# Optimization experiments

Measured on AMD Instinct MI355X. Metric: run time of the kernel, lower is better.

The kernel has to match this reference:

```python
import jax, jax.numpy as jnp
import numpy as np

DEGREE = 3        # self.degree = 3 in MGNN
K = 3             # Chebyshev/polynomial order of the GCN
BANDWIDTH = 512.0 # Gaussian kernel bandwidth (~2*d so adj spans (0,1])
B, N, D_IN = 2, 4096, 256
D_OUT = 64        # 2*D_OUT == 128 == linear output dim


def _bspline(t, degree):
    """Cox-de Boor recursive B-spline basis N_{0,degree}(t), elementwise,
    uniform knots on [0,1]. t: [B,N,N] adjacency values."""
    knots = np.linspace(0.0, 1.0, degree + 2)  # static python floats
    basis = [jnp.where((t >= knots[i]) & (t < knots[i + 1]), 1.0, 0.0).astype(t.dtype)
             for i in range(degree + 1)]
    for k in range(1, degree + 1):
        basis = [
            (t - knots[i]) / (knots[i + k] - knots[i]) * basis[i]
            + (knots[i + k + 1] - t) / (knots[i + k + 1] - knots[i + 1]) * basis[i + 1]
            for i in range(degree + 1 - k)
        ]
    return basis[0]


def _wavelet(t, degree):
    # spline wavelet: difference of dilated/shifted B-splines
    return _bspline(2.0 * t, degree) - _bspline(2.0 * t - 1.0, degree)


def _graph_construction(x, bandwidth):
    # Gaussian-kernel dense adjacency per batch element: [B,N,N], values in (0,1]
    sq = jnp.sum(x * x, axis=-1)                                   # [B,N]
    d2 = sq[:, :, None] + sq[:, None, :] - 2.0 * jnp.einsum('bnd,bmd->bnm', x, x)
    d2 = jnp.maximum(d2, 0.0)
    return jnp.exp(-d2 / bandwidth)


def _gcn(x, kernel, Wk):
    # out = sum_k (kernel^k x) W_k ; Wk: [K, D_IN, D_OUT]
    h = x
    out = jnp.einsum('bnd,do->bno', h, Wk[0])
    for k in range(1, Wk.shape[0]):
        h = jnp.einsum('bnm,bmd->bnd', kernel, h)
        out = out + jnp.einsum('bnd,do->bno', h, Wk[k])
    return out


def setup_inputs() -> dict:
    key = jax.random.key(0)
    k0, k1, k2, k3 = jax.random.split(key, 4)
    x = jax.random.normal(k0, (B, N, D_IN), dtype=jnp.float32)
    Wk = jax.random.normal(k1, (K, D_IN, D_OUT), dtype=jnp.float32) * 0.05
    W_lin = jax.random.normal(k2, (D_IN, 2 * D_OUT), dtype=jnp.float32) * 0.05
    b_lin = jnp.zeros((2 * D_OUT,), dtype=jnp.float32)
    return {"x": x, "Wk": Wk, "W_lin": W_lin, "b_lin": b_lin}


def reference(x, Wk, W_lin, b_lin):
    adj = _graph_construction(x, BANDWIDTH)       # [B,N,N]
    b_kernel = _bspline(adj, DEGREE)              # [B,N,N]
    w_kernel = _wavelet(adj, DEGREE)              # [B,N,N]
    gcn1 = _gcn(x, b_kernel, Wk)                  # [B,N,D_OUT]
    gcn2 = _gcn(x, w_kernel, Wk)                  # [B,N,D_OUT]
    akgcn = jnp.concatenate([gcn1, gcn2], axis=-1)        # [B,N,2*D_OUT]
    akgcn = jax.nn.relu(akgcn + x @ W_lin + b_lin)        # residual + relu
    return akgcn.reshape(akgcn.shape[0], -1)              # flatten last two dims
```

## Files before the change

### kernel.cpp

```cpp
#include <hip/hip_runtime.h>
#include <hip/hip_bf16.h>

typedef __hip_bfloat16 bf16;
typedef float v4f __attribute__((ext_vector_type(4)));
typedef short v8s __attribute__((ext_vector_type(8)));

typedef const __attribute__((address_space(1))) void gvoid;
typedef __attribute__((address_space(3))) void lvoid;

__device__ __forceinline__ void async16(const void* g, void* l) {
  __builtin_amdgcn_global_load_lds((gvoid*)g, (lvoid*)l, 16, 0, 0);
}

__device__ __forceinline__ unsigned short f2bf(float v) {
  __hip_bfloat16 h = __float2bfloat16(v);
  return *(unsigned short*)&h;
}
__device__ __forceinline__ float bflo(unsigned dw) {
  unsigned u = dw << 16;
  return *(float*)&u;
}
__device__ __forceinline__ float bfhi(unsigned dw) {
  unsigned u = dw & 0xffff0000u;
  return *(float*)&u;
}

__device__ __forceinline__ float b3(float u) {
  u = fminf(fmaxf(u, 0.f), 4.f);
  float t1 = fmaxf(u - 1.f, 0.f);
  float t2 = fmaxf(u - 2.f, 0.f);
  float t3 = fmaxf(u - 3.f, 0.f);
  float c0 = u * u * u;
  float c1 = t1 * t1 * t1;
  float c2 = t2 * t2 * t2;
  float c3 = t3 * t3 * t3;
  return (c0 - 4.f * c1 + 6.f * c2 - 4.f * c3) * (1.f / 6.f);
}

template <int NI, int BK>
__device__ __forceinline__ void mfma_loop(const bf16* __restrict__ A,
                                          const bf16* __restrict__ B, int lda,
                                          int ldb, int kLen, bf16* As, bf16* Bs,
                                          v4f acc[4][NI]) {
  const int tid = threadIdx.x;
  const int wave = tid >> 6;
  const int lane = tid & 63;
  const int quad = lane >> 4;
  const int r16 = lane & 15;
  const int wm = (wave >> 1) * 64;
  const int wn = (wave & 1) * (NI * 16);
  constexpr int CPR = BK / 8;
  constexpr int AQ = 128 * CPR / 256;
  constexpr int BQ = NI * 32 * CPR / 256;
  char* AsC = (char*)As;
  char* BsC = (char*)Bs;
  for (int kk = 0; kk < kLen; kk += BK) {
#pragma unroll
    for (int q = 0; q < AQ; ++q) {
      const int ch = tid + 256 * q;
      const int r = ch / CPR, c = (ch % CPR) * 8;
      async16(A + (size_t)r * lda + kk + c, AsC + q * 4096 + wave * 1024);
    }
#pragma unroll
    for (int q = 0; q < BQ; ++q) {
      const int ch = tid + 256 * q;
      const int r = ch / CPR, c = (ch % CPR) * 8;
      async16(B + (size_t)r * ldb + kk + c, BsC + q * 4096 + wave * 1024);
    }
    __syncthreads();
#pragma unroll
    for (int ks = 0; ks < BK / 32; ++ks) {
      v8s af[4], bfr[NI];
#pragma unroll
      for (int mi = 0; mi < 4; ++mi)
        af[mi] =
            *(const v8s*)(As + (wm + mi * 16 + r16) * BK + ks * 32 + quad * 8);
#pragma unroll
      for (int ni = 0; ni < NI; ++ni)
        bfr[ni] =
            *(const v8s*)(Bs + (wn + ni * 16 + r16) * BK + ks * 32 + quad * 8);
#pragma unroll
      for (int mi = 0; mi < 4; ++mi)
#pragma unroll
        for (int ni = 0; ni < NI; ++ni)
          acc[mi][ni] = __builtin_amdgcn_mfma_f32_16x16x32_bf16(
              af[mi], bfr[ni], acc[mi][ni], 0, 0, 0);
    }
    __syncthreads();
  }
}

__global__ void prep(const float* __restrict__ x, bf16* __restrict__ U,
                     float* __restrict__ sq) {
  const int n = blockIdx.x, b = blockIdx.y, t = threadIdx.x;
  const size_t row = (size_t)b * 4096 + n;
  float v = x[row * 256 + t];
  U[row * 1280 + t] = __float2bfloat16(v);
  float s = v * v;
#pragma unroll
  for (int o = 32; o > 0; o >>= 1) s += __shfl_down(s, o, 64);
  __shared__ float ls[4];
  if ((t & 63) == 0) ls[t >> 6] = s;
  __syncthreads();
  if (t == 0) sq[row] = ls[0] + ls[1] + ls[2] + ls[3];
}

__global__ void transk(const float* __restrict__ src, bf16* __restrict__ dst) {
  __shared__ float tile[64][65];
  const int z = blockIdx.z;
  const float* s = src + (size_t)z * 4096 * 256;
  bf16* d = dst + (size_t)z * 256 * 4096;
  const int n0 = blockIdx.x * 64, d0 = blockIdx.y * 64;
  const int tx = threadIdx.x & 31, ty = threadIdx.x >> 5;
#pragma unroll
  for (int i = 0; i < 8; ++i) {
    const int r = ty + i * 8;
    const float2 v = *(const float2*)(s + (size_t)(n0 + r) * 256 + d0 + tx * 2);
    tile[r][tx * 2] = v.x;
    tile[r][tx * 2 + 1] = v.y;
  }
  __syncthreads();
#pragma unroll
  for (int i = 0; i < 8; ++i) {
    const int c = ty + i * 8;
    __hip_bfloat162 p;
    p.x = __float2bfloat16(tile[tx * 2][c]);
    p.y = __float2bfloat16(tile[tx * 2 + 1][c]);
    *(__hip_bfloat162*)(d + (size_t)(d0 + c) * 4096 + n0 + tx * 2) = p;
  }
}

__global__ void wbig(const float* __restrict__ Wk, const float* __restrict__ Wl,
                     bf16* __restrict__ WbT) {
  int idx = blockIdx.x * 256 + threadIdx.x;
  if (idx >= 128 * 1280) return;
  int j = idx / 1280, k = idx % 1280;
  int o = j & 63;
  float v = 0.f;
  if (k < 256)
    v = Wk[k * 64 + o] + Wl[k * 128 + j];
  else if (k < 512)
    v = (j < 64) ? Wk[16384 + (k - 256) * 64 + o] : 0.f;
  else if (k < 768)
    v = (j < 64) ? Wk[32768 + (k - 512) * 64 + o] : 0.f;
  else if (k < 1024)
    v = (j >= 64) ? Wk[16384 + (k - 768) * 64 + o] : 0.f;
  else
    v = (j >= 64) ? Wk[32768 + (k - 1024) * 64 + o] : 0.f;
  WbT[idx] = __float2bfloat16(v);
}

__global__ __launch_bounds__(256, 2) void gemm_s(const bf16* __restrict__ U,
                                                 const float* __restrict__ sq,
                                                 bf16* __restrict__ kmat) {
  __shared__ __align__(16) bf16 As[128 * 64];
  __shared__ __align__(16) bf16 Bs[128 * 64];
  __shared__ unsigned lut[2048];
  const int tid = threadIdx.x;
  for (int i = tid; i < 2048; i += 256) {
    float t = (i + 0.5f) * (1.f / 2048.f);
    float bv = b3(4.f * t);
    float wv = b3(8.f * t) - b3(8.f * t - 4.f);
    lut[i] = (unsigned)f2bf(bv) | ((unsigned)f2bf(wv) << 16);
  }
  const int z = blockIdx.z;
  const bf16* A = U + (size_t)z * 4096 * 1280 + (size_t)blockIdx.x * 128 * 1280;
  const bf16* B = U + (size_t)z * 4096 * 1280 + (size_t)blockIdx.y * 128 * 1280;
  v4f acc[4][4];
#pragma unroll
  for (int a = 0; a < 4; ++a)
#pragma unroll
    for (int b2 = 0; b2 < 4; ++b2) acc[a][b2] = (v4f){0.f, 0.f, 0.f, 0.f};
  mfma_loop<4, 64>(A, B, 1280, 1280, 256, As, Bs, acc);
  const int wave = tid >> 6, lane = tid & 63;
  const int quad = lane >> 4, r16 = lane & 15;
  const int wm = (wave >> 1) * 64, wn = (wave & 1) * 64;
  const float* sqr = sq + (size_t)z * 4096;
  unsigned short* bk = (unsigned short*)(kmat + (size_t)(z * 2) * 4096 * 4096);
  unsigned short* wk = bk + (size_t)4096 * 4096;
  const int i0 = blockIdx.x * 128 + wm + quad * 4;
  const int j0 = blockIdx.y * 128 + wn + r16;
  const int par = lane & 1;
  const int jc = j0 - par;
  float sqj[4];
#pragma unroll
  for (int ni = 0; ni < 4; ++ni) sqj[ni] = sqr[j0 + ni * 16];
  const float c = -1.4426950408889634f / 512.f;
#pragma unroll
  for (int mi = 0; mi < 4; ++mi) {
#pragma unroll
    for (int ni = 0; ni < 4; ++ni) {
      unsigned pv[4];
#pragma unroll
      for (int r = 0; r < 4; ++r) {
        float s = acc[mi][ni][r];
        float d2 = fmaxf(sqr[i0 + mi * 16 + r] + sqj[ni] - 2.f * s, 0.f);
        float t = __builtin_amdgcn_exp2f(d2 * c);
        int idx = (int)fminf(t * 2048.f, 2047.f);
        pv[r] = lut[idx];
      }
      unsigned ov[4];
#pragma unroll
      for (int r = 0; r < 4; ++r) ov[r] = __shfl_xor((int)pv[r], 1, 64);
#pragma unroll
      for (int rr = 0; rr < 2; ++rr) {
        const int r = par * 2 + rr;
        const unsigned a = pv[r], b2 = ov[r];
        const unsigned lo = par ? b2 : a;
        const unsigned hi = par ? a : b2;
        const unsigned bkd = (lo & 0xffffu) | (hi << 16);
        const unsigned wkd = (lo >> 16) | (hi & 0xffff0000u);
        const int i = i0 + mi * 16 + r;
        const size_t off = (size_t)i * 4096 + jc + ni * 16;
        *(unsigned*)(bk + off) = bkd;
        *(unsigned*)(wk + off) = wkd;
      }
    }
  }
}

__global__ __launch_bounds__(256, 4) void gemm_h(const bf16* __restrict__ kmat,
                                                 const bf16* __restrict__ BtBase,
                                                 bf16* __restrict__ hpart,
                                                 int btShift) {
  __shared__ __align__(16) bf16 As[128 * 64];
  __shared__ __align__(16) bf16 Bs[128 * 64];
  const int bz = blockIdx.z;
  const int z = bz >> 2, split = bz & 3;
  const int kk0 = split * 1024;
  const bf16* A =
      kmat + (size_t)z * 4096 * 4096 + (size_t)blockIdx.x * 128 * 4096 + kk0;
  const bf16* B = BtBase + (size_t)(z >> btShift) * 256 * 4096 +
                  (size_t)blockIdx.y * 128 * 4096 + kk0;
  v4f acc[4][4];
#pragma unroll
  for (int a = 0; a < 4; ++a)
#pragma unroll
    for (int b2 = 0; b2 < 4; ++b2) acc[a][b2] = (v4f){0.f, 0.f, 0.f, 0.f};
  mfma_loop<4, 64>(A, B, 4096, 4096, 1024, As, Bs, acc);
  const int tid = threadIdx.x, wave = tid >> 6, lane = tid & 63;
  const int quad = lane >> 4, r16 = lane & 15;
  const int wm = (wave >> 1) * 64, wn = (wave & 1) * 64;
  bf16* H = hpart + ((size_t)split * 4 + z) * 4096 * 256;
  const int i0 = blockIdx.x * 128 + wm + quad * 4;
  const int j0 = blockIdx.y * 128 + wn + r16;
  const int par = lane & 1;
  const int jc = j0 - par;
#pragma unroll
  for (int mi = 0; mi < 4; ++mi) {
#pragma unroll
    for (int ni = 0; ni < 4; ++ni) {
      unsigned pv[4];
#pragma unroll
      for (int r = 0; r < 4; ++r) pv[r] = (unsigned)f2bf(acc[mi][ni][r]);
      unsigned ov[4];
#pragma unroll
      for (int r = 0; r < 4; ++r) ov[r] = __shfl_xor((int)pv[r], 1, 64);
#pragma unroll
      for (int rr = 0; rr < 2; ++rr) {
        const int r = par * 2 + rr;
        const unsigned a = pv[r], b2 = ov[r];
        const unsigned lo = par ? b2 : a;
        const unsigned hi = par ? a : b2;
        const int i = i0 + mi * 16 + r;
        *(unsigned*)(H + (size_t)i * 256 + jc + ni * 16) = lo | (hi << 16);
      }
    }
  }
}

__global__ void reduceT(const bf16* __restrict__ hpart, bf16* __restrict__ U,
                        bf16* __restrict__ hT, int uoffBase) {
  __shared__ float tile[64][65];
  const int z = blockIdx.z;
  const int b = z >> 1, kern = z & 1;
  const int uoff = uoffBase + kern * 512;
  const int n0 = blockIdx.x * 64, d0 = blockIdx.y * 64;
  const int tx = threadIdx.x & 31, ty = threadIdx.x >> 5;
  const size_t sstride = (size_t)4 * 4096 * 256;
  const bf16* s0 = hpart + (size_t)z * 4096 * 256;
#pragma unroll
  for (int i = 0; i < 8; ++i) {
    const int r = ty + i * 8;
    const size_t off = (size_t)(n0 + r) * 256 + d0 + tx * 2;
    float vx = 0.f, vy = 0.f;
#pragma unroll
    for (int k = 0; k < 4; ++k) {
      const unsigned dw = *(const unsigned*)(s0 + k * sstride + off);
      vx += bflo(dw);
      vy += bfhi(dw);
    }
    tile[r][tx * 2] = vx;
    tile[r][tx * 2 + 1] = vy;
    __hip_bfloat162 p;
    p.x = __float2bfloat16(vx);
    p.y = __float2bfloat16(vy);
    *(__hip_bfloat162*)(U + (size_t)(b * 4096 + n0 + r) * 1280 + uoff + d0 +
                        tx * 2) = p;
  }
  if (hT) {
    __syncthreads();
#pragma unroll
    for (int i = 0; i < 8; ++i) {
      const int c = ty + i * 8;
      __hip_bfloat162 p;
      p.x = __float2bfloat16(tile[tx * 2][c]);
      p.y = __float2bfloat16(tile[tx * 2 + 1][c]);
      *(__hip_bfloat162*)(hT + (size_t)z * 256 * 4096 + (size_t)(d0 + c) * 4096 +
                          n0 + tx * 2) = p;
    }
  }
}

__global__ __launch_bounds__(256, 4) void gemm_proj(
    const bf16* __restrict__ U, const bf16* __restrict__ WbT,
    const float* __restrict__ blin, float* __restrict__ out) {
  __shared__ __align__(16) bf16 As[128 * 64];
  __shared__ __align__(16) bf16 Bs[64 * 64];
  const bf16* A = U + (size_t)blockIdx.x * 128 * 1280;
  const bf16* B = WbT + (size_t)blockIdx.y * 64 * 1280;
  v4f acc[4][2];
#pragma unroll
  for (int a = 0; a < 4; ++a)
#pragma unroll
    for (int b2 = 0; b2 < 2; ++b2) acc[a][b2] = (v4f){0.f, 0.f, 0.f, 0.f};
  mfma_loop<2, 64>(A, B, 1280, 1280, 1280, As, Bs, acc);
  const int tid = threadIdx.x, wave = tid >> 6, lane = tid & 63;
  const int quad = lane >> 4, r16 = lane & 15;
  const int wm = (wave >> 1) * 64, wn = (wave & 1) * 32;
  const int i0 = blockIdx.x * 128 + wm + quad * 4;
  const int j0 = blockIdx.y * 64 + wn + r16;
#pragma unroll
  for (int mi = 0; mi < 4; ++mi)
#pragma unroll
    for (int r = 0; r < 4; ++r) {
      const int i = i0 + mi * 16 + r;
#pragma unroll
      for (int ni = 0; ni < 2; ++ni) {
        const int j = j0 + ni * 16;
        out[(size_t)i * 128 + j] = fmaxf(acc[mi][ni][r] + blin[j], 0.f);
      }
    }
}

extern "C" void kernel_launch(void* const* d_in, const int* in_sizes, int n_in,
                              void* d_out, int out_size, void* d_ws,
                              size_t ws_size, hipStream_t stream) {
  const float* x = (const float*)d_in[0];
  const float* Wk = (const float*)d_in[1];
  const float* Wlin = (const float*)d_in[2];
  const float* blin = (const float*)d_in[3];
  float* out = (float*)d_out;
  char* w = (char*)d_ws;
  bf16* kmat = (bf16*)(w);
  bf16* hpart = (bf16*)(w + 134217728);
  bf16* h1T = (bf16*)(w + 201326592);
  bf16* xhT = (bf16*)(w + 209715200);
  bf16* U = (bf16*)(w + 213909504);
  bf16* WbT = (bf16*)(w + 234881024);
  float* sqv = (float*)(w + 235208704);

  prep<<<dim3(4096, 2), 256, 0, stream>>>(x, U, sqv);
  transk<<<dim3(64, 4, 2), 256, 0, stream>>>(x, xhT);
  wbig<<<dim3(640), 256, 0, stream>>>(Wk, Wlin, WbT);
  gemm_s<<<dim3(32, 32, 2), 256, 0, stream>>>(U, sqv, kmat);
  gemm_h<<<dim3(32, 2, 16), 256, 0, stream>>>(kmat, xhT, hpart, 1);
  reduceT<<<dim3(64, 4, 4), 256, 0, stream>>>(hpart, U, h1T, 256);
  gemm_h<<<dim3(32, 2, 16), 256, 0, stream>>>(kmat, h1T, hpart, 0);
  reduceT<<<dim3(64, 4, 4), 256, 0, stream>>>(hpart, U, nullptr, 512);
  gemm_proj<<<dim3(64, 2), 256, 0, stream>>>(U, WbT, blin, out);
}
```

Baseline: 245.7 us.

## Fuse adjacency construction with kernel-times-features GEMM to avoid materializing kernel matrix

Replaces the separate kernel-matrix GEMM and the two propagation GEMMs with one fused kernel. It computes Gaussian distances, does the B-spline/wavelet LUT lookup into shared memory tiles, and multiplies directly against the feature matrix. This removes writing and re-reading the large bf16 kernel matrices from global memory. In exchange, the Gram computation is redone for each propagation hop, and the kernel uses large shared memory with no double buffering, which limits occupancy.

```diff
diff --git a/kernel.cpp b/kernel.cpp
--- a/kernel.cpp
+++ b/kernel.cpp
@@ -150,120 +150,197 @@
   WbT[idx] = __float2bfloat16(v);
 }
 
-__global__ __launch_bounds__(256, 2) void gemm_s(const bf16* __restrict__ U,
-                                                 const float* __restrict__ sq,
-                                                 bf16* __restrict__ kmat) {
-  __shared__ __align__(16) bf16 As[128 * 64];
-  __shared__ __align__(16) bf16 Bs[128 * 64];
+__global__ __launch_bounds__(512, 2) void fused_kh(
+    const bf16* __restrict__ U, const float* __restrict__ sqv,
+    const bf16* __restrict__ VbB, const bf16* __restrict__ VwB, int bmul,
+    bf16* __restrict__ hpart) {
+  __shared__ __align__(16) bf16 Xi[64 * 256];
+  __shared__ __align__(16) bf16 Xj[128 * 128];
+  __shared__ __align__(16) bf16 Pb[64 * 128];
+  __shared__ __align__(16) bf16 Pw[64 * 128];
+  __shared__ __align__(16) bf16 Vt[256 * 64];
   __shared__ unsigned lut[2048];
+
   const int tid = threadIdx.x;
-  for (int i = tid; i < 2048; i += 256) {
+  const int wave = tid >> 6, lane = tid & 63;
+  const int quad = lane >> 4, r16 = lane & 15;
+  const int par = lane & 1;
+  const int wm = (wave >> 2) * 32;
+  const int wns = (wave & 3) * 32;
+  const int wnp = (wave & 3) * 64;
+  const int i0 = blockIdx.x * 64;
+  const int split = blockIdx.y;
+  const int b = blockIdx.z;
+
+  for (int i = tid; i < 2048; i += 512) {
     float t = (i + 0.5f) * (1.f / 2048.f);
     float bv = b3(4.f * t);
     float wv = b3(8.f * t) - b3(8.f * t - 4.f);
     lut[i] = (unsigned)f2bf(bv) | ((unsigned)f2bf(wv) << 16);
   }
-  const int z = blockIdx.z;
-  const bf16* A = U + (size_t)z * 4096 * 1280 + (size_t)blockIdx.x * 128 * 1280;
-  const bf16* B = U + (size_t)z * 4096 * 1280 + (size_t)blockIdx.y * 128 * 1280;
-  v4f acc[4][4];
-#pragma unroll
-  for (int a = 0; a < 4; ++a)
-#pragma unroll
-    for (int b2 = 0; b2 < 4; ++b2) acc[a][b2] = (v4f){0.f, 0.f, 0.f, 0.f};
-  mfma_loop<4, 64>(A, B, 1280, 1280, 256, As, Bs, acc);
-  const int wave = tid >> 6, lane = tid & 63;
-  const int quad = lane >> 4, r16 = lane & 15;
-  const int wm = (wave >> 1) * 64, wn = (wave & 1) * 64;
-  const float* sqr = sq + (size_t)z * 4096;
-  unsigned short* bk = (unsigned short*)(kmat + (size_t)(z * 2) * 4096 * 4096);
-  unsigned short* wk = bk + (size_t)4096 * 4096;
-  const int i0 = blockIdx.x * 128 + wm + quad * 4;
-  const int j0 = blockIdx.y * 128 + wn + r16;
-  const int par = lane & 1;
-  const int jc = j0 - par;
-  float sqj[4];
-#pragma unroll
-  for (int ni = 0; ni < 4; ++ni) sqj[ni] = sqr[j0 + ni * 16];
-  const float c = -1.4426950408889634f / 512.f;
-#pragma unroll
-  for (int mi = 0; mi < 4; ++mi) {
-#pragma unroll
-    for (int ni = 0; ni < 4; ++ni) {
-      unsigned pv[4];
-#pragma unroll
-      for (int r = 0; r < 4; ++r) {
-        float s = acc[mi][ni][r];
-        float d2 = fmaxf(sqr[i0 + mi * 16 + r] + sqj[ni] - 2.f * s, 0.f);
-        float t = __builtin_amdgcn_exp2f(d2 * c);
-        int idx = (int)fminf(t * 2048.f, 2047.f);
-        pv[r] = lut[idx];
-      }
-      unsigned ov[4];
-#pragma unroll
-      for (int r = 0; r < 4; ++r) ov[r] = __shfl_xor((int)pv[r], 1, 64);
-#pragma unroll
-      for (int rr = 0; rr < 2; ++rr) {
-        const int r = par * 2 + rr;
-        const unsigned a = pv[r], b2 = ov[r];
-        const unsigned lo = par ? b2 : a;
-        const unsigned hi = par ? a : b2;
-        const unsigned bkd = (lo & 0xffffu) | (hi << 16);
-        const unsigned wkd = (lo >> 16) | (hi & 0xffff0000u);
-        const int i = i0 + mi * 16 + r;
-        const size_t off = (size_t)i * 4096 + jc + ni * 16;
-        *(unsigned*)(bk + off) = bkd;
-        *(unsigned*)(wk + off) = wkd;
-      }
-    }
-  }
-}
-
-__global__ __launch_bounds__(256, 4) void gemm_h(const bf16* __restrict__ kmat,
-                                                 const bf16* __restrict__ BtBase,
-                                                 bf16* __restrict__ hpart,
-                                                 int btShift) {
-  __shared__ __align__(16) bf16 As[128 * 64];
-  __shared__ __align__(16) bf16 Bs[128 * 64];
-  const int bz = blockIdx.z;
-  const int z = bz >> 2, split = bz & 3;
-  const int kk0 = split * 1024;
-  const bf16* A =
-      kmat + (size_t)z * 4096 * 4096 + (size_t)blockIdx.x * 128 * 4096 + kk0;
-  const bf16* B = BtBase + (size_t)(z >> btShift) * 256 * 4096 +
-                  (size_t)blockIdx.y * 128 * 4096 + kk0;
-  v4f acc[4][4];
-#pragma unroll
-  for (int a = 0; a < 4; ++a)
-#pragma unroll
-    for (int b2 = 0; b2 < 4; ++b2) acc[a][b2] = (v4f){0.f, 0.f, 0.f, 0.f};
-  mfma_loop<4, 64>(A, B, 4096, 4096, 1024, As, Bs, acc);
-  const int tid = threadIdx.x, wave = tid >> 6, lane = tid & 63;
-  const int quad = lane >> 4, r16 = lane & 15;
-  const int wm = (wave >> 1) * 64, wn = (wave & 1) * 64;
-  bf16* H = hpart + ((size_t)split * 4 + z) * 4096 * 256;
-  const int i0 = blockIdx.x * 128 + wm + quad * 4;
-  const int j0 = blockIdx.y * 128 + wn + r16;
-  const int par = lane & 1;
-  const int jc = j0 - par;
-#pragma unroll
-  for (int mi = 0; mi < 4; ++mi) {
-#pragma unroll
-    for (int ni = 0; ni < 4; ++ni) {
-      unsigned pv[4];
-#pragma unroll
-      for (int r = 0; r < 4; ++r) pv[r] = (unsigned)f2bf(acc[mi][ni][r]);
-      unsigned ov[4];
-#pragma unroll
-      for (int r = 0; r < 4; ++r) ov[r] = __shfl_xor((int)pv[r], 1, 64);
-#pragma unroll
-      for (int rr = 0; rr < 2; ++rr) {
-        const int r = par * 2 + rr;
-        const unsigned a = pv[r], b2 = ov[r];
-        const unsigned lo = par ? b2 : a;
-        const unsigned hi = par ? a : b2;
-        const int i = i0 + mi * 16 + r;
-        *(unsigned*)(H + (size_t)i * 256 + jc + ni * 16) = lo | (hi << 16);
+
+  {
+    char* XiC = (char*)Xi;
+    const bf16* src = U + (size_t)(b * 4096 + i0) * 1280;
+#pragma unroll
+    for (int q = 0; q < 4; ++q) {
+      const int ch = tid + 512 * q;
+      const int r = ch >> 5, c = (ch & 31) * 8;
+      async16(src + (size_t)r * 1280 + c, XiC + q * 8192 + wave * 1024);
+    }
+  }
+
+  const float* sqr = sqv + b * 4096;
+  float sqi[8];
+#pragma unroll
+  for (int mi = 0; mi < 2; ++mi)
+#pragma unroll
+    for (int r = 0; r < 4; ++r)
+      sqi[mi * 4 + r] = sqr[i0 + wm + mi * 16 + quad * 4 + r];
+
+  v4f acc[2][2][4];
+#pragma unroll
+  for (int k2 = 0; k2 < 2; ++k2)
+#pragma unroll
+    for (int mi = 0; mi < 2; ++mi)
+#pragma unroll
+      for (int ni = 0; ni < 4; ++ni) acc[k2][mi][ni] = (v4f){0.f, 0.f, 0.f, 0.f};
+
+  const bf16* Vb = VbB + (size_t)b * bmul * 256 * 4096;
+  const bf16* Vw = VwB + (size_t)b * bmul * 256 * 4096;
+  const float cexp = -1.4426950408889634f / 512.f;
+
+  for (int jt = 0; jt < 8; ++jt) {
+    const int j0g = split * 1024 + jt * 128;
+    v4f accs[2][2];
+#pragma unroll
+    for (int mi = 0; mi < 2; ++mi)
+#pragma unroll
+      for (int ni = 0; ni < 2; ++ni) accs[mi][ni] = (v4f){0.f, 0.f, 0.f, 0.f};
+    char* XjC = (char*)Xj;
+    const bf16* bsrc = U + (size_t)(b * 4096 + j0g) * 1280;
+#pragma unroll
+    for (int kh = 0; kh < 2; ++kh) {
+#pragma unroll
+      for (int q = 0; q < 4; ++q) {
+        const int ch = tid + 512 * q;
+        const int r = ch >> 4, c = (ch & 15) * 8;
+        async16(bsrc + (size_t)r * 1280 + kh * 128 + c,
+                XjC + q * 8192 + wave * 1024);
+      }
+      __syncthreads();
+#pragma unroll
+      for (int ks = 0; ks < 4; ++ks) {
+        v8s af[2], bfr[2];
+#pragma unroll
+        for (int mi = 0; mi < 2; ++mi)
+          af[mi] = *(const v8s*)(Xi + (wm + mi * 16 + r16) * 256 + kh * 128 +
+                                 ks * 32 + quad * 8);
+#pragma unroll
+        for (int ni = 0; ni < 2; ++ni)
+          bfr[ni] = *(const v8s*)(Xj + (wns + ni * 16 + r16) * 128 + ks * 32 +
+                                  quad * 8);
+#pragma unroll
+        for (int mi = 0; mi < 2; ++mi)
+#pragma unroll
+          for (int ni = 0; ni < 2; ++ni)
+            accs[mi][ni] = __builtin_amdgcn_mfma_f32_16x16x32_bf16(
+                af[mi], bfr[ni], accs[mi][ni], 0, 0, 0);
+      }
+      if (kh == 0) __syncthreads();
+    }
+    float sqj[2];
+#pragma unroll
+    for (int ni = 0; ni < 2; ++ni) sqj[ni] = sqr[j0g + wns + ni * 16 + r16];
+#pragma unroll
+    for (int mi = 0; mi < 2; ++mi) {
+#pragma unroll
+      for (int ni = 0; ni < 2; ++ni) {
+        unsigned pv[4];
+#pragma unroll
+        for (int r = 0; r < 4; ++r) {
+          float s = accs[mi][ni][r];
+          float d2 = fmaxf(sqi[mi * 4 + r] + sqj[ni] - 2.f * s, 0.f);
+          float t = __builtin_amdgcn_exp2f(d2 * cexp);
+          int idx = (int)fminf(t * 2048.f, 2047.f);
+          pv[r] = lut[idx];
+        }
+        unsigned ov[4];
+#pragma unroll
+        for (int r = 0; r < 4; ++r) ov[r] = __shfl_xor((int)pv[r], 1, 64);
+#pragma unroll
+        for (int rr = 0; rr < 2; ++rr) {
+          const int r = par * 2 + rr;
+          const unsigned ea = pv[r], eb = ov[r];
+          const unsigned lo = par ? eb : ea;
+          const unsigned hi = par ? ea : eb;
+          const int row = wm + mi * 16 + quad * 4 + r;
+          const int colp = wns + ni * 16 + (r16 & ~1);
+          *(unsigned*)(Pb + row * 128 + colp) = (lo & 0xffffu) | (hi << 16);
+          *(unsigned*)(Pw + row * 128 + colp) =
+              (lo >> 16) | (hi & 0xffff0000u);
+        }
+      }
+    }
+    __syncthreads();
+    char* VtC = (char*)Vt;
+#pragma unroll
+    for (int kv = 0; kv < 4; ++kv) {
+      const int kern = kv >> 1, jh = kv & 1;
+      const bf16* vsrc = (kern ? Vw : Vb) + j0g + jh * 64;
+#pragma unroll
+      for (int q = 0; q < 4; ++q) {
+        const int ch = tid + 512 * q;
+        const int r = ch >> 3, c = (ch & 7) * 8;
+        async16(vsrc + (size_t)r * 4096 + c, VtC + q * 8192 + wave * 1024);
+      }
+      __syncthreads();
+      const bf16* P = kern ? Pw : Pb;
+#pragma unroll
+      for (int ks = 0; ks < 2; ++ks) {
+        v8s pa[2], bv[4];
+#pragma unroll
+        for (int mi = 0; mi < 2; ++mi)
+          pa[mi] = *(const v8s*)(P + (wm + mi * 16 + r16) * 128 + jh * 64 +
+                                 ks * 32 + quad * 8);
+#pragma unroll
+        for (int ni = 0; ni < 4; ++ni)
+          bv[ni] = *(const v8s*)(Vt + (wnp + ni * 16 + r16) * 64 + ks * 32 +
+                                 quad * 8);
+#pragma unroll
+        for (int mi = 0; mi < 2; ++mi)
+#pragma unroll
+          for (int ni = 0; ni < 4; ++ni)
+            acc[kern][mi][ni] = __builtin_amdgcn_mfma_f32_16x16x32_bf16(
+                pa[mi], bv[ni], acc[kern][mi][ni], 0, 0, 0);
+      }
+      __syncthreads();
+    }
+  }
+#pragma unroll
+  for (int kern = 0; kern < 2; ++kern) {
+    bf16* H = hpart + ((size_t)split * 4 + b * 2 + kern) * 4096 * 256;
+#pragma unroll
+    for (int mi = 0; mi < 2; ++mi) {
+#pragma unroll
+      for (int ni = 0; ni < 4; ++ni) {
+        unsigned pv[4];
+#pragma unroll
+        for (int r = 0; r < 4; ++r)
+          pv[r] = (unsigned)f2bf(acc[kern][mi][ni][r]);
+        unsigned ov[4];
+#pragma unroll
+        for (int r = 0; r < 4; ++r) ov[r] = __shfl_xor((int)pv[r], 1, 64);
+#pragma unroll
+        for (int rr = 0; rr < 2; ++rr) {
+          const int r = par * 2 + rr;
+          const unsigned ea = pv[r], eb = ov[r];
+          const unsigned lo = par ? eb : ea;
+          const unsigned hi = par ? ea : eb;
+          const int i = i0 + wm + mi * 16 + quad * 4 + r;
+          const int colp = wnp + ni * 16 + (r16 & ~1);
+          *(unsigned*)(H + (size_t)i * 256 + colp) = lo | (hi << 16);
+        }
       }
     }
   }
@@ -352,21 +429,20 @@
   const float* blin = (const float*)d_in[3];
   float* out = (float*)d_out;
   char* w = (char*)d_ws;
-  bf16* kmat = (bf16*)(w);
-  bf16* hpart = (bf16*)(w + 134217728);
-  bf16* h1T = (bf16*)(w + 201326592);
-  bf16* xhT = (bf16*)(w + 209715200);
-  bf16* U = (bf16*)(w + 213909504);
-  bf16* WbT = (bf16*)(w + 234881024);
-  float* sqv = (float*)(w + 235208704);
+  bf16* hpart = (bf16*)(w);
+  bf16* h1T = (bf16*)(w + 33554432);
+  bf16* xhT = (bf16*)(w + 41943040);
+  bf16* U = (bf16*)(w + 46137344);
+  bf16* WbT = (bf16*)(w + 67108864);
+  float* sqv = (float*)(w + 67436544);
 
   prep<<<dim3(4096, 2), 256, 0, stream>>>(x, U, sqv);
   transk<<<dim3(64, 4, 2), 256, 0, stream>>>(x, xhT);
   wbig<<<dim3(640), 256, 0, stream>>>(Wk, Wlin, WbT);
-  gemm_s<<<dim3(32, 32, 2), 256, 0, stream>>>(U, sqv, kmat);
-  gemm_h<<<dim3(32, 2, 16), 256, 0, stream>>>(kmat, xhT, hpart, 1);
+  fused_kh<<<dim3(64, 4, 2), 512, 0, stream>>>(U, sqv, xhT, xhT, 1, hpart);
   reduceT<<<dim3(64, 4, 4), 256, 0, stream>>>(hpart, U, h1T, 256);
-  gemm_h<<<dim3(32, 2, 16), 256, 0, stream>>>(kmat, h1T, hpart, 0);
+  fused_kh<<<dim3(64, 4, 2), 512, 0, stream>>>(
+      U, sqv, h1T, h1T + (size_t)256 * 4096, 2, hpart);
   reduceT<<<dim3(64, 4, 4), 256, 0, stream>>>(hpart, U, nullptr, 512);
   gemm_proj<<<dim3(64, 2), 256, 0, stream>>>(U, WbT, blin, out);
 }
```

After: 500.3 us. 2.04x slower.

## Widen gemm_h tile to cover all 256 output columns with 512-thread blocks

Applied to the files above, without the earlier changes.

Each gemm_h block now computes a 128x256 output tile using 8 waves instead of 128x128 with 4 waves, halving the grid along y. This makes each A-tile of the large kernel matrix load from global memory once instead of twice, cutting the dominant read traffic. The shared mfma_loop helper is replaced by an inline single-buffered load/sync/compute loop, which may lose any latency hiding the helper provided and reduces the number of blocks and occupancy.

```diff
diff --git a/kernel.cpp b/kernel.cpp
--- a/kernel.cpp
+++ b/kernel.cpp
@@ -219,31 +219,66 @@
   }
 }
 
-__global__ __launch_bounds__(256, 4) void gemm_h(const bf16* __restrict__ kmat,
+__global__ __launch_bounds__(512, 2) void gemm_h(const bf16* __restrict__ kmat,
                                                  const bf16* __restrict__ BtBase,
                                                  bf16* __restrict__ hpart,
                                                  int btShift) {
   __shared__ __align__(16) bf16 As[128 * 64];
-  __shared__ __align__(16) bf16 Bs[128 * 64];
+  __shared__ __align__(16) bf16 Bs[256 * 64];
   const int bz = blockIdx.z;
   const int z = bz >> 2, split = bz & 3;
   const int kk0 = split * 1024;
   const bf16* A =
       kmat + (size_t)z * 4096 * 4096 + (size_t)blockIdx.x * 128 * 4096 + kk0;
-  const bf16* B = BtBase + (size_t)(z >> btShift) * 256 * 4096 +
-                  (size_t)blockIdx.y * 128 * 4096 + kk0;
-  v4f acc[4][4];
-#pragma unroll
-  for (int a = 0; a < 4; ++a)
-#pragma unroll
-    for (int b2 = 0; b2 < 4; ++b2) acc[a][b2] = (v4f){0.f, 0.f, 0.f, 0.f};
-  mfma_loop<4, 64>(A, B, 4096, 4096, 1024, As, Bs, acc);
+  const bf16* B = BtBase + (size_t)(z >> btShift) * 256 * 4096 + kk0;
   const int tid = threadIdx.x, wave = tid >> 6, lane = tid & 63;
   const int quad = lane >> 4, r16 = lane & 15;
-  const int wm = (wave >> 1) * 64, wn = (wave & 1) * 64;
+  const int wm = (wave >> 2) * 64;
+  const int wn = (wave & 3) * 64;
+  char* AsC = (char*)As;
+  char* BsC = (char*)Bs;
+  v4f acc[4][4];
+#pragma unroll
+  for (int a = 0; a < 4; ++a)
+#pragma unroll
+    for (int b2 = 0; b2 < 4; ++b2) acc[a][b2] = (v4f){0.f, 0.f, 0.f, 0.f};
+  for (int kk = 0; kk < 1024; kk += 64) {
+#pragma unroll
+    for (int q = 0; q < 2; ++q) {
+      const int ch = tid + 512 * q;
+      const int r = ch >> 3, c = (ch & 7) * 8;
+      async16(A + (size_t)r * 4096 + kk + c, AsC + q * 8192 + wave * 1024);
+    }
+#pragma unroll
+    for (int q = 0; q < 4; ++q) {
+      const int ch = tid + 512 * q;
+      const int r = ch >> 3, c = (ch & 7) * 8;
+      async16(B + (size_t)r * 4096 + kk + c, BsC + q * 8192 + wave * 1024);
+    }
+    __syncthreads();
+#pragma unroll
+    for (int ks = 0; ks < 2; ++ks) {
+      v8s af[4], bfr[4];
+#pragma unroll
+      for (int mi = 0; mi < 4; ++mi)
+        af[mi] =
+            *(const v8s*)(As + (wm + mi * 16 + r16) * 64 + ks * 32 + quad * 8);
+#pragma unroll
+      for (int ni = 0; ni < 4; ++ni)
+        bfr[ni] =
+            *(const v8s*)(Bs + (wn + ni * 16 + r16) * 64 + ks * 32 + quad * 8);
+#pragma unroll
+      for (int mi = 0; mi < 4; ++mi)
+#pragma unroll
+        for (int ni = 0; ni < 4; ++ni)
+          acc[mi][ni] = __builtin_amdgcn_mfma_f32_16x16x32_bf16(
+              af[mi], bfr[ni], acc[mi][ni], 0, 0, 0);
+    }
+    __syncthreads();
+  }
   bf16* H = hpart + ((size_t)split * 4 + z) * 4096 * 256;
   const int i0 = blockIdx.x * 128 + wm + quad * 4;
-  const int j0 = blockIdx.y * 128 + wn + r16;
+  const int j0 = wn + r16;
   const int par = lane & 1;
   const int jc = j0 - par;
 #pragma unroll
@@ -364,9 +399,9 @@
   transk<<<dim3(64, 4, 2), 256, 0, stream>>>(x, xhT);
   wbig<<<dim3(640), 256, 0, stream>>>(Wk, Wlin, WbT);
   gemm_s<<<dim3(32, 32, 2), 256, 0, stream>>>(U, sqv, kmat);
-  gemm_h<<<dim3(32, 2, 16), 256, 0, stream>>>(kmat, xhT, hpart, 1);
+  gemm_h<<<dim3(32, 1, 16), 512, 0, stream>>>(kmat, xhT, hpart, 1);
   reduceT<<<dim3(64, 4, 4), 256, 0, stream>>>(hpart, U, h1T, 256);
-  gemm_h<<<dim3(32, 2, 16), 256, 0, stream>>>(kmat, h1T, hpart, 0);
+  gemm_h<<<dim3(32, 1, 16), 512, 0, stream>>>(kmat, h1T, hpart, 0);
   reduceT<<<dim3(64, 4, 4), 256, 0, stream>>>(hpart, U, nullptr, 512);
   gemm_proj<<<dim3(64, 2), 256, 0, stream>>>(U, WbT, blin, out);
 }
```

After: 248.5 us. Within noise of the previous version (+1.1%).
